# Kernel tuning notes

Measured on AMD Instinct MI355X. Metric: run time of the kernel, lower is better.

## Reference

```python
import jax, jax.numpy as jnp
import numpy as np

B, S, H = 4096, 15, 1024
PQ, CFG = 1003, 128
IN = PQ + 5 + 10 + 3 + 3  # 1024, matches input_size in torch module
EPS = 1e-5


def lstm_cell(x, h, c, Wih, Whh, bih, bhh):
    # PyTorch LSTMCell gate order: i, f, g, o
    gates = x @ Wih.T + bih + h @ Whh.T + bhh
    i, f, g, o = jnp.split(gates, 4, axis=-1)
    c2 = jax.nn.sigmoid(f) * c + jax.nn.sigmoid(i) * jnp.tanh(g)
    h2 = jax.nn.sigmoid(o) * jnp.tanh(c2)
    return h2, c2


def setup_inputs() -> dict:
    key = jax.random.key(0)
    ks = jax.random.split(key, 16)
    g = lambda i, shape, s=0.02: jax.random.normal(ks[i], shape, jnp.float32) * s
    u = lambda i, shape: jax.random.uniform(ks[i], shape, jnp.float32, -1.0, 1.0)
    return {
        "input_p_q": jax.random.normal(ks[0], (B, S, PQ), jnp.float32),
        "input_config": jax.random.normal(ks[1], (B, S, CFG), jnp.float32),
        "input_time": jax.random.randint(ks[2], (B, S, 3), 0, 5),
        "W_cfg": g(3, (10, CFG)), "b_cfg": jnp.zeros((10,), jnp.float32),
        "emb_hour": g(4, (24, 5), 1.0),
        "emb_weekday": g(5, (8, 3), 1.0),
        "emb_season": g(6, (5, 3), 1.0),
        # init(): uniform(-1,1) weights, zero bias for the two attention layers
        "W_sa": u(7, (IN, IN + 2 * H)), "b_sa": jnp.zeros((IN,), jnp.float32),
        "Wih_s": g(8, (4 * H, IN)), "Whh_s": g(9, (4 * H, H)),
        "bih_s": jnp.zeros((4 * H,), jnp.float32), "bhh_s": jnp.zeros((4 * H,), jnp.float32),
        "Wih_t": g(10, (4 * H, H)), "Whh_t": g(11, (4 * H, H)),
        "bih_t": jnp.zeros((4 * H,), jnp.float32), "bhh_t": jnp.zeros((4 * H,), jnp.float32),
        "W_ta": u(12, (1, 3 * H)), "b_ta": jnp.zeros((1,), jnp.float32),
        "bn_gamma": jnp.ones((S,), jnp.float32), "bn_beta": jnp.zeros((S,), jnp.float32),
        "Wih_d": g(13, (4, H)), "Whh_d": g(14, (4, 1)),
        "bih_d": jnp.zeros((4,), jnp.float32), "bhh_d": jnp.zeros((4,), jnp.float32),
    }


def reference(input_p_q, input_config, input_time,
              W_cfg, b_cfg, emb_hour, emb_weekday, emb_season,
              W_sa, b_sa, Wih_s, Whh_s, bih_s, bhh_s,
              Wih_t, Whh_t, bih_t, bhh_t, W_ta, b_ta,
              bn_gamma, bn_beta, Wih_d, Whh_d, bih_d, bhh_d):
    cfg = input_config @ W_cfg.T + b_cfg                       # [B,S,10]
    hr = emb_hour[input_time[:, :, 0]]                         # [B,S,5]
    wd = emb_weekday[input_time[:, :, 1]]                      # [B,S,3]
    sn = emb_season[input_time[:, :, 2]]                       # [B,S,3]
    inputs = jnp.concatenate([input_p_q, cfg, hr, wd, sn], axis=2)  # [B,S,IN]

    Bsz, Ssz = inputs.shape[0], inputs.shape[1]
    Hd = Whh_s.shape[1]
    h0 = jnp.zeros((Bsz, Hd), inputs.dtype)

    # ---- spatial encoder with per-step attention gating ----
    def step1(carry, x):
        h, c = carry
        score = jnp.tanh(jnp.concatenate([h, c, x], axis=1) @ W_sa.T + b_sa)
        h2, c2 = lstm_cell(x * score, h, c, Wih_s, Whh_s, bih_s, bhh_s)
        return (h2, c2), h2

    _, mid = jax.lax.scan(step1, (h0, h0), jnp.swapaxes(inputs, 0, 1))  # [S,B,H]
    mid = jnp.swapaxes(mid, 0, 1)                                      # [B,S,H]

    # ---- BatchNorm1d(15) in training mode: channels = sequence dim ----
    mu = mid.mean(axis=(0, 2), keepdims=True)
    var = mid.var(axis=(0, 2), keepdims=True)  # biased variance, as torch uses for normalization
    mid = (mid - mu) * jax.lax.rsqrt(var + EPS) * bn_gamma[None, :, None] + bn_beta[None, :, None]

    # ---- temporal encoder with post-step attention score ----
    def step2(carry, x):
        h, c = carry
        h2, c2 = lstm_cell(x, h, c, Wih_t, Whh_t, bih_t, bhh_t)
        att = jnp.tanh(jnp.concatenate([h2, c2, x], axis=1) @ W_ta.T + b_ta)  # [B,1]
        return (h2, c2), (h2, att)

    _, (outs, att2) = jax.lax.scan(step2, (h0, h0), jnp.swapaxes(mid, 0, 1))
    outs = jnp.swapaxes(outs, 0, 1)   # [B,S,H]
    att2 = jnp.swapaxes(att2, 0, 1)   # [B,S,1]

    # ---- decoder nn.LSTM (batch_first=False!) scans over the BATCH axis ----
    hd0 = jnp.zeros((Ssz, 1), outs.dtype)

    def step3(carry, x):
        h, c = carry
        h2, c2 = lstm_cell(x, h, c, Wih_d, Whh_d, bih_d, bhh_d)
        return (h2, c2), h2

    _, out1d = jax.lax.scan(step3, (hd0, hd0), outs)  # [B,S,1]

    sm = jax.nn.softmax(att2, axis=1)  # [B,S,1]
    # bmm(out1d^T [B,1,S], sm [B,S,1]) -> [B,1,1]
    out = jnp.einsum('bs,bs->b', out1d[:, :, 0], sm[:, :, 0])[:, None, None]
    return out
```

## Files before the change

kernel.cpp:

```cpp
#include <hip/hip_runtime.h>

#define AS1 __attribute__((address_space(1)))
#define AS3 __attribute__((address_space(3)))

typedef __attribute__((ext_vector_type(8))) _Float16 f16x8;
typedef __attribute__((ext_vector_type(4))) float f32x4;

static constexpr int BATCH = 4096;
static constexpr int SEQ   = 15;

__device__ __forceinline__ float h2f(unsigned short u) {
  return (float)__builtin_bit_cast(_Float16, u);
}
__device__ __forceinline__ unsigned short f2h(float f) {
  return __builtin_bit_cast(unsigned short, (_Float16)f);
}
__device__ __forceinline__ float frcp(float x) { return __builtin_amdgcn_rcpf(x); }
__device__ __forceinline__ float sigm(float x)  { return frcp(1.0f + __expf(-x)); }
__device__ __forceinline__ float tanhx(float x) { return 1.0f - 2.0f * frcp(1.0f + __expf(2.0f * x)); }

template<int STAGE>
__global__ __launch_bounds__(512, 2)
void gemm_lstm256(const unsigned short* A0, int lda0, int K0,
                  const unsigned short* A1, int lda1,
                  const unsigned short* Bw, int K,
                  const float* ib, float* Cst,
                  unsigned short* P0, unsigned short* P1, unsigned short* P2,
                  float* F0)
{
  __shared__ unsigned short lds[2][2][16384];
  const int tid  = threadIdx.x;
  const int wid  = tid >> 6;
  const int lane = tid & 63;
  const int wr = wid >> 2;
  const int wc = wid & 3;
  const int NT = K >> 6;

  const int bid = blockIdx.y * gridDim.x + blockIdx.x;
  const int cpx = (gridDim.x * gridDim.y) >> 3;
  const int swz = (bid & 7) * cpx + (bid >> 3);
  const int row0 = (swz / gridDim.x) * 256;
  const int col0 = (swz % gridDim.x) * 256;

  auto stage_half = [&](int bb, int mat, int hh, int kt) {
    const int k0 = kt * 64;
    const unsigned short* Ap; int lda, kc, rb;
    if (mat == 0) {
      if (k0 < K0) { Ap = A0; lda = lda0; kc = k0; }
      else         { Ap = A1; lda = lda1; kc = k0 - K0; }
      rb = row0;
    } else { Ap = Bw; lda = K; kc = k0; rb = col0; }
#pragma unroll
    for (int i = 0; i < 2; ++i) {
      const int x  = (tid + i * 512) * 16;
      const int xs = x ^ (((x >> 9) & 1) << 5);
      const int r  = hh * 128 + (xs >> 7);
      const int cb = xs & 127;
      const unsigned short* src = Ap + (size_t)(rb + r) * lda + kc + (cb >> 1);
      __builtin_amdgcn_global_load_lds((const AS1 void*)src,
          (AS3 void*)((char*)&lds[bb][mat][0] + hh * 16384 + wid * 1024 + i * 8192),
          16, 0, 0);
    }
  };

  const int frow = lane & 15;
  const int axor = ((lane >> 2) & 1) << 5;
  const int abase = ((((wr * 128 + frow) << 7) + (((lane >> 4) & 3) << 4))) ^ axor;
  const int bbase = ((((wc * 64  + frow) << 7) + (((lane >> 4) & 3) << 4))) ^ axor;

  const f32x4 zero = {0.f, 0.f, 0.f, 0.f};
  f32x4 acc[8][4];
#pragma unroll
  for (int i = 0; i < 8; ++i)
#pragma unroll
    for (int j = 0; j < 4; ++j) acc[i][j] = zero;

  stage_half(0, 0, 0, 0);
  stage_half(0, 0, 1, 0);
  stage_half(0, 1, 0, 0);
  stage_half(0, 1, 1, 0);
  if (NT > 1) { stage_half(1, 1, 0, 1); stage_half(1, 1, 1, 1); }
  asm volatile("s_waitcnt vmcnt(4)" ::: "memory");
  __builtin_amdgcn_s_barrier();

#define DO_PHASE(MB, STG, VMW)                                                        \
  {                                                                                   \
    const f16x8 a0 = *(const f16x8*)(ldsA + abase + (MB)     * 2048);                 \
    const f16x8 a1 = *(const f16x8*)(ldsA + abase + (MB)     * 2048 + 64);            \
    const f16x8 a2 = *(const f16x8*)(ldsA + abase + (MB + 1) * 2048);                 \
    const f16x8 a3 = *(const f16x8*)(ldsA + abase + (MB + 1) * 2048 + 64);            \
    STG;                                                                              \
    __builtin_amdgcn_s_barrier();                                                     \
    asm volatile("s_waitcnt lgkmcnt(0)" ::: "memory");                                \
    __builtin_amdgcn_sched_barrier(0);                                                \
    __builtin_amdgcn_s_setprio(1);                                                    \
    _Pragma("unroll")                                                                 \
    for (int n = 0; n < 4; ++n) {                                                     \
      acc[MB][n]     = __builtin_amdgcn_mfma_f32_16x16x32_f16(a0, bv[n][0], acc[MB][n],     0, 0, 0); \
      acc[MB][n]     = __builtin_amdgcn_mfma_f32_16x16x32_f16(a1, bv[n][1], acc[MB][n],     0, 0, 0); \
      acc[MB + 1][n] = __builtin_amdgcn_mfma_f32_16x16x32_f16(a2, bv[n][0], acc[MB + 1][n], 0, 0, 0); \
      acc[MB + 1][n] = __builtin_amdgcn_mfma_f32_16x16x32_f16(a3, bv[n][1], acc[MB + 1][n], 0, 0, 0); \
    }                                                                                 \
    __builtin_amdgcn_s_setprio(0);                                                    \
    VMW;                                                                              \
    __builtin_amdgcn_s_barrier();                                                     \
  }

  for (int kt = 0; kt < NT; ++kt) {
    const int cur = kt & 1;
    const char* ldsA = (const char*)&lds[cur][0][0];
    const char* ldsB = (const char*)&lds[cur][1][0];
    f16x8 bv[4][2];
#pragma unroll
    for (int n = 0; n < 4; ++n) {
      bv[n][0] = *(const f16x8*)(ldsB + bbase + n * 2048);
      bv[n][1] = *(const f16x8*)(ldsB + bbase + n * 2048 + 64);
    }
    DO_PHASE(0, { if (kt + 1 < NT) stage_half(cur ^ 1, 0, 0, kt + 1); }, { (void)0; });
    DO_PHASE(2, { if (kt + 1 < NT) stage_half(cur ^ 1, 0, 1, kt + 1); }, { (void)0; });
    DO_PHASE(4, { if (kt + 2 < NT) stage_half(cur,     1, 0, kt + 2); }, { (void)0; });
    DO_PHASE(6, { if (kt + 2 < NT) stage_half(cur,     1, 1, kt + 2); },
             { if (kt >= NT - 2) { asm volatile("s_waitcnt vmcnt(0)" ::: "memory"); }
               else              { asm volatile("s_waitcnt vmcnt(4)" ::: "memory"); } });
  }
#undef DO_PHASE

  __syncthreads();
  char* base = (char*)&lds[0][0][0];
  unsigned short* hS = (unsigned short*)base;
  unsigned short* cS = (unsigned short*)(base + 32768);
  float*          hF = (float*)base;
  float* xw = (float*)(base + 65536) + wid * 256;

  const int cs = lane & 3;
  const int er = (lane >> 4) << 2;
  const int uq = (lane >> 2) & 3;

  float cold[8][4];
#pragma unroll
  for (int mi = 0; mi < 8; ++mi)
#pragma unroll
    for (int ni = 0; ni < 4; ++ni) {
      const int R = row0 + wr * 128 + mi * 16 + er + cs;
      const int U = ((col0 + wc * 64 + ni * 16) >> 2) + uq;
      cold[mi][ni] = Cst[(size_t)R * 1024 + U];
    }

#pragma unroll
  for (int mi = 0; mi < 8; ++mi)
#pragma unroll
    for (int ni = 0; ni < 4; ++ni) {
      __builtin_amdgcn_wave_barrier();
      *(f32x4*)(xw + lane * 4) = acc[mi][ni];
      __builtin_amdgcn_wave_barrier();
      __builtin_amdgcn_sched_barrier(0);
      const int qb = (lane & 60) * 4;
      const float g0 = xw[qb + 0  + cs];
      const float g1 = xw[qb + 4  + cs];
      const float g2 = xw[qb + 8  + cs];
      const float g3 = xw[qb + 12 + cs];
      __builtin_amdgcn_wave_barrier();
      const int R = row0 + wr * 128 + mi * 16 + er + cs;
      const int U = ((col0 + wc * 64 + ni * 16) >> 2) + uq;
      const f32x4 b4 = *(const f32x4*)(ib + 4 * U);
      const float gi = g0 + b4[0];
      const float gf = g1 + b4[1];
      const float gg = g2 + b4[2];
      const float go = g3 + b4[3];
      const float cn = sigm(gf) * cold[mi][ni] + sigm(gi) * tanhx(gg);
      const float hn = sigm(go) * tanhx(cn);
      Cst[(size_t)R * 1024 + U] = cn;
      const int Rl = wr * 128 + mi * 16 + er + cs;
      const int Ul = wc * 16 + ni * 4 + uq;
      if (STAGE == 1) {
        hS[Rl * 64 + Ul] = f2h(hn);
        cS[Rl * 64 + Ul] = f2h(cn);
      } else {
        hF[Rl * 64 + Ul] = hn;
      }
    }
  __syncthreads();

  const int U0 = col0 >> 2;
  if (STAGE == 1) {
#pragma unroll
    for (int it = 0; it < 4; ++it) {
      const int idx = it * 512 + tid;
      const int r = idx >> 3, o = idx & 7;
      const int4 hv = *(const int4*)((char*)hS + idx * 16);
      const int4 cv = *(const int4*)((char*)cS + idx * 16);
      *(int4*)(P0 + (size_t)(row0 + r) * 2048 + U0 + o * 8)        = hv;
      *(int4*)(P0 + (size_t)(row0 + r) * 2048 + 1024 + U0 + o * 8) = cv;
      *(int4*)(P1 + (size_t)(row0 + r) * 2048 + 1024 + U0 + o * 8) = hv;
      *(int4*)(P2 + (size_t)(row0 + r) * 1024 + U0 + o * 8)        = hv;
    }
  } else {
#pragma unroll
    for (int it = 0; it < 8; ++it) {
      const int idx = it * 512 + tid;
      const int r = idx >> 4, o = idx & 15;
      const f32x4 hv = *(const f32x4*)((char*)hF + idx * 16);
      *(f32x4*)(F0 + (size_t)(row0 + r) * 1024 + U0 + o * 4) = hv;
      uint2 pk;
      pk.x = (unsigned)f2h(hv[0]) | ((unsigned)f2h(hv[1]) << 16);
      pk.y = (unsigned)f2h(hv[2]) | ((unsigned)f2h(hv[3]) << 16);
      *(uint2*)(P0 + (size_t)(row0 + r) * 1024 + U0 + o * 4) = pk;
    }
  }
}

__global__ __launch_bounds__(256, 2)
void gemm_score2ph(const unsigned short* A0, int lda0, int K0,
                   const unsigned short* A1, int lda1,
                   const unsigned short* Bw, int K,
                   const float* bias, const unsigned short* X,
                   unsigned short* OutG)
{
  __shared__ unsigned short lds[2][12288];
  const int tid  = threadIdx.x;
  const int wid  = tid >> 6;
  const int lane = tid & 63;
  const int wr = wid >> 1;
  const int wc = wid & 1;
  const int NT = K >> 6;

  const int bid = blockIdx.y * gridDim.x + blockIdx.x;
  const int cpx = (gridDim.x * gridDim.y) >> 3;
  const int swz = (bid & 7) * cpx + (bid >> 3);
  const int row0 = (swz / gridDim.x) * 128;
  const int col0 = (swz % gridDim.x) * 64;

  auto stage_A = [&](int bb, int kt) {
    const int k0 = kt * 64;
    const unsigned short* Ap; int lda, kc;
    if (k0 < K0) { Ap = A0; lda = lda0; kc = k0; }
    else         { Ap = A1; lda = lda1; kc = k0 - K0; }
#pragma unroll
    for (int i = 0; i < 4; ++i) {
      const int x  = (i * 256 + tid) * 16;
      const int xs = x ^ (((x >> 9) & 1) << 5);
      const int r  = xs >> 7;
      const int cb = xs & 127;
      const unsigned short* src = Ap + (size_t)(row0 + r) * lda + kc + (cb >> 1);
      __builtin_amdgcn_global_load_lds((const AS1 void*)src,
          (AS3 void*)((char*)&lds[bb][0] + i * 4096 + wid * 1024), 16, 0, 0);
    }
  };
  auto stage_B = [&](int bb, int kt) {
    const int k0 = kt * 64;
#pragma unroll
    for (int i = 0; i < 2; ++i) {
      const int x  = (i * 256 + tid) * 16;
      const int xs = x ^ (((x >> 9) & 1) << 5);
      const int r  = xs >> 7;
      const int cb = xs & 127;
      const unsigned short* src = Bw + (size_t)(col0 + r) * K + k0 + (cb >> 1);
      __builtin_amdgcn_global_load_lds((const AS1 void*)src,
          (AS3 void*)((char*)&lds[bb][0] + 16384 + i * 4096 + wid * 1024), 16, 0, 0);
    }
  };

  const int frow = lane & 15;
  const int axor = ((lane >> 2) & 1) << 5;
  const int abase = ((((wr * 64 + frow) << 7) + ((lane >> 4) << 4))) ^ axor;
  const int bbase = ((((wc * 32 + frow) << 7) + ((lane >> 4) << 4))) ^ axor;

  const f32x4 zero = {0.f, 0.f, 0.f, 0.f};
  f32x4 acc[4][2];
#pragma unroll
  for (int i = 0; i < 4; ++i)
#pragma unroll
    for (int j = 0; j < 2; ++j) acc[i][j] = zero;

  stage_A(0, 0);
  stage_B(0, 0);
  if (NT > 1) stage_B(1, 1);
  asm volatile("s_waitcnt vmcnt(2)" ::: "memory");
  __builtin_amdgcn_s_barrier();

  for (int kt = 0; kt < NT; ++kt) {
    const int cur = kt & 1;
    const char* ldsA = (const char*)&lds[cur][0];
    const char* ldsB = ldsA + 16384;
    f16x8 bv[2][2];
#pragma unroll
    for (int n = 0; n < 2; ++n) {
      bv[n][0] = *(const f16x8*)(ldsB + bbase + n * 2048);
      bv[n][1] = *(const f16x8*)(ldsB + bbase + n * 2048 + 64);
    }
    f16x8 a00 = *(const f16x8*)(ldsA + abase);
    f16x8 a01 = *(const f16x8*)(ldsA + abase + 64);
    f16x8 a10 = *(const f16x8*)(ldsA + abase + 2048);
    f16x8 a11 = *(const f16x8*)(ldsA + abase + 2048 + 64);
    if (kt + 1 < NT) stage_A(cur ^ 1, kt + 1);
    __builtin_amdgcn_s_barrier();
    asm volatile("s_waitcnt lgkmcnt(0)" ::: "memory");
    __builtin_amdgcn_sched_barrier(0);
    __builtin_amdgcn_s_setprio(1);
#pragma unroll
    for (int n = 0; n < 2; ++n) {
      acc[0][n] = __builtin_amdgcn_mfma_f32_16x16x32_f16(a00, bv[n][0], acc[0][n], 0, 0, 0);
      acc[0][n] = __builtin_amdgcn_mfma_f32_16x16x32_f16(a01, bv[n][1], acc[0][n], 0, 0, 0);
      acc[1][n] = __builtin_amdgcn_mfma_f32_16x16x32_f16(a10, bv[n][0], acc[1][n], 0, 0, 0);
      acc[1][n] = __builtin_amdgcn_mfma_f32_16x16x32_f16(a11, bv[n][1], acc[1][n], 0, 0, 0);
    }
    __builtin_amdgcn_s_setprio(0);
    __builtin_amdgcn_s_barrier();
    f16x8 a20 = *(const f16x8*)(ldsA + abase + 2 * 2048);
    f16x8 a21 = *(const f16x8*)(ldsA + abase + 2 * 2048 + 64);
    f16x8 a30 = *(const f16x8*)(ldsA + abase + 3 * 2048);
    f16x8 a31 = *(const f16x8*)(ldsA + abase + 3 * 2048 + 64);
    if (kt + 2 < NT) stage_B(cur, kt + 2);
    __builtin_amdgcn_s_barrier();
    asm volatile("s_waitcnt lgkmcnt(0)" ::: "memory");
    __builtin_amdgcn_sched_barrier(0);
    __builtin_amdgcn_s_setprio(1);
#pragma unroll
    for (int n = 0; n < 2; ++n) {
      acc[2][n] = __builtin_amdgcn_mfma_f32_16x16x32_f16(a20, bv[n][0], acc[2][n], 0, 0, 0);
      acc[2][n] = __builtin_amdgcn_mfma_f32_16x16x32_f16(a21, bv[n][1], acc[2][n], 0, 0, 0);
      acc[3][n] = __builtin_amdgcn_mfma_f32_16x16x32_f16(a30, bv[n][0], acc[3][n], 0, 0, 0);
      acc[3][n] = __builtin_amdgcn_mfma_f32_16x16x32_f16(a31, bv[n][1], acc[3][n], 0, 0, 0);
    }
    __builtin_amdgcn_s_setprio(0);
    if (kt >= NT - 2) { asm volatile("s_waitcnt vmcnt(0)" ::: "memory"); }
    else              { asm volatile("s_waitcnt vmcnt(2)" ::: "memory"); }
    __builtin_amdgcn_s_barrier();
  }

  const int er = (lane >> 4) << 2;
#pragma unroll
  for (int mi = 0; mi < 4; ++mi)
#pragma unroll
    for (int ni = 0; ni < 2; ++ni) {
      const int row = row0 + wr * 64 + mi * 16 + er;
      const int col = col0 + wc * 32 + ni * 16 + frow;
      const float bs = bias[col];
#pragma unroll
      for (int r = 0; r < 4; ++r) {
        const float v = tanhx(acc[mi][ni][r] + bs);
        const float xv = h2f(X[(size_t)(row + r) * 1024 + col]);
        OutG[(size_t)(row + r) * 2048 + col] = f2h(xv * v);
      }
    }
}

__global__ void f2h_copy(const float* src, unsigned short* dst, int n) {
  const int i = blockIdx.x * 256 + threadIdx.x;
  if (i < n) dst[i] = f2h(src[i]);
}

__global__ void cat_w_int(const float* wih, const float* whh, unsigned short* dst) {
  const int i = blockIdx.x * 256 + threadIdx.x;
  const int n = i >> 11, k = i & 2047;
  const int u = n >> 2, g = n & 3;
  const int src = g * 1024 + u;
  dst[i] = f2h(k < 1024 ? wih[src * 1024 + k] : whh[src * 1024 + (k - 1024)]);
}

__global__ void prep_bias(const float* bih, const float* bhh, float* ib) {
  const int i = blockIdx.x * 256 + threadIdx.x;
  const int u = i >> 2, g = i & 3;
  ib[i] = bih[g * 1024 + u] + bhh[g * 1024 + u];
}

__global__ void copy_pq(const float* pq, unsigned short* inb) {
  const int i4 = blockIdx.x * 256 + threadIdx.x;
  const float4 v = ((const float4*)pq)[i4];
  const int base = i4 * 4;
  const float vv[4] = {v.x, v.y, v.z, v.w};
#pragma unroll
  for (int e = 0; e < 4; ++e) {
    const int idx = base + e;
    const int bt = idx / 1003;
    const int j = idx - bt * 1003;
    const int b = bt / 15;
    const int t = bt - b * 15;
    inb[((size_t)t * BATCH + b) * 1024 + j] = f2h(vv[e]);
  }
}

__global__ void cfg_emb(const float* cfg, const int* tim,
                        const float* Wc, const float* bc,
                        const float* eh, const float* ew, const float* es,
                        unsigned short* inb)
{
  const int wv = (blockIdx.x * 256 + threadIdx.x) >> 6;
  const int lane = threadIdx.x & 63;
  const int b = wv / 15, t = wv - b * 15;
  const float* cp = cfg + (size_t)wv * 128;
  const float c0 = cp[lane], c1v = cp[lane + 64];
  unsigned short* dst = inb + ((size_t)t * BATCH + b) * 1024;
#pragma unroll
  for (int g = 0; g < 10; ++g) {
    float v = fmaf(c0, Wc[g * 128 + lane], c1v * Wc[g * 128 + 64 + lane]);
    v += __shfl_xor(v, 32); v += __shfl_xor(v, 16); v += __shfl_xor(v, 8);
    v += __shfl_xor(v, 4);  v += __shfl_xor(v, 2);  v += __shfl_xor(v, 1);
    if (lane == 0) dst[1003 + g] = f2h(v + bc[g]);
  }
  if (lane < 5)       dst[1013 + lane] = f2h(eh[tim[wv * 3 + 0] * 5 + lane]);
  else if (lane < 8)  dst[1018 + (lane - 5)] = f2h(ew[tim[wv * 3 + 1] * 3 + (lane - 5)]);
  else if (lane < 11) dst[1021 + (lane - 8)] = f2h(es[tim[wv * 3 + 2] * 3 + (lane - 8)]);
}

__global__ void bn_partial(const unsigned short* mid, float* part) {
  const int t = blockIdx.y, blk = blockIdx.x, tid = threadIdx.x;
  const unsigned short* p = mid + (size_t)t * BATCH * 1024;
  float s = 0.f, ss = 0.f;
  for (int i = blk * 256 + tid; i < BATCH * 1024; i += 128 * 256) {
    const float v = h2f(p[i]);
    s += v; ss += v * v;
  }
  for (int o = 32; o > 0; o >>= 1) { s += __shfl_down(s, o); ss += __shfl_down(ss, o); }
  __shared__ float sm[8];
  if ((tid & 63) == 0) { sm[(tid >> 6) * 2] = s; sm[(tid >> 6) * 2 + 1] = ss; }
  __syncthreads();
  if (tid == 0) {
    part[(t * 128 + blk) * 2]     = sm[0] + sm[2] + sm[4] + sm[6];
    part[(t * 128 + blk) * 2 + 1] = sm[1] + sm[3] + sm[5] + sm[7];
  }
}

__global__ void bn_final(const float* part, const float* gamma, const float* beta, float* scsh) {
  const int t = blockIdx.x, tid = threadIdx.x;
  float s = part[(t * 128 + tid) * 2], ss = part[(t * 128 + tid) * 2 + 1];
  for (int o = 32; o > 0; o >>= 1) { s += __shfl_down(s, o); ss += __shfl_down(ss, o); }
  __shared__ float sm[4];
  if ((tid & 63) == 0) { sm[(tid >> 6) * 2] = s; sm[(tid >> 6) * 2 + 1] = ss; }
  __syncthreads();
  if (tid == 0) {
    const float S = sm[0] + sm[2], SS = sm[1] + sm[3];
    const float inv = 1.f / (float)(BATCH * 1024);
    const float mu = S * inv;
    const float var = SS * inv - mu * mu;
    const float rstd = rsqrtf(var + 1e-5f);
    const float sc = rstd * gamma[t];
    scsh[t * 2] = sc;
    scsh[t * 2 + 1] = beta[t] - mu * sc;
  }
}

__global__ void bn_apply(unsigned short* mid, const float* scsh) {
  const int t = blockIdx.y;
  const int i = blockIdx.x * 256 + threadIdx.x;
  unsigned short* p = mid + (size_t)t * BATCH * 1024;
  p[i] = f2h(h2f(p[i]) * scsh[t * 2] + scsh[t * 2 + 1]);
}

__global__ void att_proj(const float* h2, const float* c2, const unsigned short* xn,
                         const float* Wta, const float* bta, const float* Wihd,
                         float* att2, float* proj, int t)
{
  const int b = blockIdx.x, tid = threadIdx.x;
  const float* h = h2 + (size_t)b * 1024;
  const float* c = c2 + (size_t)b * 1024;
  const unsigned short* x = xn + (size_t)b * 1024;
  float a = 0.f, p0 = 0.f, p1 = 0.f, p2 = 0.f, p3 = 0.f;
  for (int j = tid; j < 1024; j += 256) {
    const float hv = h[j], cv = c[j], xv = h2f(x[j]);
    a  += hv * Wta[j] + cv * Wta[1024 + j] + xv * Wta[2048 + j];
    p0 += hv * Wihd[j];
    p1 += hv * Wihd[1024 + j];
    p2 += hv * Wihd[2048 + j];
    p3 += hv * Wihd[3072 + j];
  }
  for (int o = 32; o > 0; o >>= 1) {
    a  += __shfl_down(a, o);  p0 += __shfl_down(p0, o); p1 += __shfl_down(p1, o);
    p2 += __shfl_down(p2, o); p3 += __shfl_down(p3, o);
  }
  __shared__ float sm[4][5];
  if ((tid & 63) == 0) {
    const int w = tid >> 6;
    sm[w][0] = a; sm[w][1] = p0; sm[w][2] = p1; sm[w][3] = p2; sm[w][4] = p3;
  }
  __syncthreads();
  if (tid == 0) {
    att2[b * SEQ + t] = tanhx(sm[0][0] + sm[1][0] + sm[2][0] + sm[3][0] + bta[0]);
    float* pp = proj + ((size_t)b * SEQ + t) * 4;
    pp[0] = sm[0][1] + sm[1][1] + sm[2][1] + sm[3][1];
    pp[1] = sm[0][2] + sm[1][2] + sm[2][2] + sm[3][2];
    pp[2] = sm[0][3] + sm[1][3] + sm[2][3] + sm[3][3];
    pp[3] = sm[0][4] + sm[1][4] + sm[2][4] + sm[3][4];
  }
}

__global__ __launch_bounds__(256) void lstm3_par(
    const float* proj, const float* Whhd,
    const float* bihd, const float* bhhd, float* out1d)
{
  const int s = blockIdx.x;
  const int tid = threadIdx.x;
  constexpr int CH = BATCH / 256;
  const float wi = Whhd[0], wf = Whhd[1], wg = Whhd[2], wo = Whhd[3];
  const float bi = bihd[0] + bhhd[0], bf_ = bihd[1] + bhhd[1];
  const float bg = bihd[2] + bhhd[2], bo = bihd[3] + bhhd[3];
  const float4* p4 = (const float4*)proj;
  float4 p[CH];
#pragma unroll
  for (int u = 0; u < CH; ++u) p[u] = p4[(tid * CH + u) * SEQ + s];
  __shared__ float Hb[257], Cb[257];
  Hb[tid] = 0.f; Cb[tid] = 0.f;
  if (tid == 255) { Hb[256] = 0.f; Cb[256] = 0.f; }
  __syncthreads();
  float h, c;
  for (int it = 0; it < 8; ++it) {
    h = Hb[tid]; c = Cb[tid];
#pragma unroll
    for (int u = 0; u < CH; ++u) {
      const float gi = fmaf(h, wi, p[u].x + bi);
      const float gf = fmaf(h, wf, p[u].y + bf_);
      const float gg = fmaf(h, wg, p[u].z + bg);
      const float go = fmaf(h, wo, p[u].w + bo);
      c = sigm(gf) * c + sigm(gi) * tanhx(gg);
      h = sigm(go) * tanhx(c);
    }
    __syncthreads();
    Hb[tid + 1] = h; Cb[tid + 1] = c;
    __syncthreads();
  }
  h = Hb[tid]; c = Cb[tid];
#pragma unroll
  for (int u = 0; u < CH; ++u) {
    const float gi = fmaf(h, wi, p[u].x + bi);
    const float gf = fmaf(h, wf, p[u].y + bf_);
    const float gg = fmaf(h, wg, p[u].z + bg);
    const float go = fmaf(h, wo, p[u].w + bo);
    c = sigm(gf) * c + sigm(gi) * tanhx(gg);
    h = sigm(go) * tanhx(c);
    out1d[(tid * CH + u) * SEQ + s] = h;
  }
}

__global__ void finalize_k(const float* att2, const float* out1d, float* out) {
  const int b = blockIdx.x * 64 + threadIdx.x;
  const float* a = att2 + b * SEQ;
  const float* o = out1d + b * SEQ;
  float m = -1e30f;
  for (int s = 0; s < SEQ; ++s) m = fmaxf(m, a[s]);
  float den = 0.f, num = 0.f;
  for (int s = 0; s < SEQ; ++s) {
    const float e = __expf(a[s] - m);
    den += e; num += e * o[s];
  }
  out[b] = num / den;
}

extern "C" void kernel_launch(void* const* d_in, const int* in_sizes, int n_in,
                              void* d_out, int out_size, void* d_ws, size_t ws_size,
                              hipStream_t stream)
{
  (void)in_sizes; (void)n_in; (void)out_size; (void)ws_size;
  const float* in_pq   = (const float*)d_in[0];
  const float* in_cfg  = (const float*)d_in[1];
  const int*   in_time = (const int*)d_in[2];
  const float* W_cfg   = (const float*)d_in[3];
  const float* b_cfg   = (const float*)d_in[4];
  const float* emb_h   = (const float*)d_in[5];
  const float* emb_w   = (const float*)d_in[6];
  const float* emb_s   = (const float*)d_in[7];
  const float* W_sa    = (const float*)d_in[8];
  const float* b_sa    = (const float*)d_in[9];
  const float* Wih_s   = (const float*)d_in[10];
  const float* Whh_s   = (const float*)d_in[11];
  const float* bih_s   = (const float*)d_in[12];
  const float* bhh_s   = (const float*)d_in[13];
  const float* Wih_t   = (const float*)d_in[14];
  const float* Whh_t   = (const float*)d_in[15];
  const float* bih_t   = (const float*)d_in[16];
  const float* bhh_t   = (const float*)d_in[17];
  const float* W_ta    = (const float*)d_in[18];
  const float* b_ta    = (const float*)d_in[19];
  const float* gamma   = (const float*)d_in[20];
  const float* beta    = (const float*)d_in[21];
  const float* Wih_d   = (const float*)d_in[22];
  const float* Whh_d   = (const float*)d_in[23];
  const float* bih_d   = (const float*)d_in[24];
  const float* bhh_d   = (const float*)d_in[25];
  float* out = (float*)d_out;

  char* w = (char*)d_ws;
  size_t off = 0;
  auto alloc = [&](size_t bytes) -> char* {
    char* p = w + off;
    off = (off + bytes + 255) & ~(size_t)255;
    return p;
  };
  unsigned short* inb  = (unsigned short*)alloc((size_t)SEQ * BATCH * 1024 * 2);
  unsigned short* hc   = (unsigned short*)alloc((size_t)BATCH * 2048 * 2);
  unsigned short* gA0  = (unsigned short*)alloc((size_t)BATCH * 2048 * 2);
  unsigned short* gA1  = (unsigned short*)alloc((size_t)BATCH * 2048 * 2);
  float*          c1   = (float*)alloc((size_t)BATCH * 1024 * 4);
  unsigned short* h2b0 = (unsigned short*)alloc((size_t)BATCH * 1024 * 2);
  unsigned short* h2b1 = (unsigned short*)alloc((size_t)BATCH * 1024 * 2);
  float*          h2f_ = (float*)alloc((size_t)BATCH * 1024 * 4);
  float*          c2f  = (float*)alloc((size_t)BATCH * 1024 * 4);
  unsigned short* wsab = (unsigned short*)alloc((size_t)1024 * 3072 * 2);
  unsigned short* w1   = (unsigned short*)alloc((size_t)4096 * 2048 * 2);
  unsigned short* w2   = (unsigned short*)alloc((size_t)4096 * 2048 * 2);
  float*          ib1  = (float*)alloc(4096 * 4);
  float*          ib2  = (float*)alloc(4096 * 4);
  float*          part = (float*)alloc(15 * 128 * 2 * 4);
  float*          scsh = (float*)alloc(15 * 2 * 4);
  float*          att2 = (float*)alloc((size_t)BATCH * SEQ * 4);
  float*          proj = (float*)alloc((size_t)BATCH * SEQ * 4 * 4);
  float*          o1d  = (float*)alloc((size_t)BATCH * SEQ * 4);

  unsigned short* gAbuf[2]  = {gA0, gA1};
  unsigned short* h2bbuf[2] = {h2b0, h2b1};

  hipMemsetAsync(hc,   0, (size_t)BATCH * 2048 * 2, stream);
  hipMemsetAsync(gA0,  0, (size_t)BATCH * 2048 * 2, stream);
  hipMemsetAsync(c1,   0, (size_t)BATCH * 1024 * 4, stream);
  hipMemsetAsync(h2b0, 0, (size_t)BATCH * 1024 * 2, stream);
  hipMemsetAsync(c2f,  0, (size_t)BATCH * 1024 * 4, stream);

  f2h_copy<<<(1024 * 3072) / 256, 256, 0, stream>>>(W_sa, wsab, 1024 * 3072);
  cat_w_int<<<(4096 * 2048) / 256, 256, 0, stream>>>(Wih_s, Whh_s, w1);
  cat_w_int<<<(4096 * 2048) / 256, 256, 0, stream>>>(Wih_t, Whh_t, w2);
  prep_bias<<<16, 256, 0, stream>>>(bih_s, bhh_s, ib1);
  prep_bias<<<16, 256, 0, stream>>>(bih_t, bhh_t, ib2);
  copy_pq<<<(BATCH * SEQ * 1003 / 4) / 256, 256, 0, stream>>>(in_pq, inb);
  cfg_emb<<<(BATCH * SEQ) / 4, 256, 0, stream>>>(in_cfg, in_time, W_cfg, b_cfg,
                                                 emb_h, emb_w, emb_s, inb);

  for (int t = 0; t < SEQ; ++t) {
    unsigned short* xt = inb + (size_t)t * BATCH * 1024;
    gemm_score2ph<<<dim3(1024 / 64, BATCH / 128), 256, 0, stream>>>(
        hc, 2048, 2048, xt, 1024, wsab, 3072, b_sa, xt, gAbuf[t & 1]);
    gemm_lstm256<1><<<dim3(4096 / 256, BATCH / 256), 512, 0, stream>>>(
        gAbuf[t & 1], 2048, 2048, gAbuf[t & 1], 2048, w1, 2048,
        ib1, c1, hc, gAbuf[(t + 1) & 1], xt, nullptr);
  }

  bn_partial<<<dim3(128, SEQ), 256, 0, stream>>>(inb, part);
  bn_final<<<SEQ, 128, 0, stream>>>(part, gamma, beta, scsh);
  bn_apply<<<dim3((BATCH * 1024) / 256, SEQ), 256, 0, stream>>>(inb, scsh);

  for (int t = 0; t < SEQ; ++t) {
    const unsigned short* xt = inb + (size_t)t * BATCH * 1024;
    gemm_lstm256<2><<<dim3(4096 / 256, BATCH / 256), 512, 0, stream>>>(
        xt, 1024, 1024, h2bbuf[t & 1], 1024, w2, 2048,
        ib2, c2f, h2bbuf[(t + 1) & 1], nullptr, nullptr, h2f_);
    att_proj<<<BATCH, 256, 0, stream>>>(h2f_, c2f, xt, W_ta, b_ta, Wih_d, att2, proj, t);
  }

  lstm3_par<<<SEQ, 256, 0, stream>>>(proj, Whh_d, bih_d, bhh_d, o1d);
  finalize_k<<<BATCH / 64, 64, 0, stream>>>(att2, o1d, out);
}
```

Baseline: 3.544 ms.

## Fuse attention score and decoder projection dot products into temporal LSTM epilogue

The stage-2 LSTM GEMM epilogue now computes per-row partial dot products of h and c with the attention weights and the decoder input weights while the values are still in registers. It writes these 16 column-block partials to a buffer instead of storing an fp32 copy of h. A single reduction kernel after the loop sums them, and a separate batched kernel precomputes the x·W_ta term across all timesteps. This removes the per-step att_proj kernel, which reread fp32 h and c from global memory, at the cost of extra epilogue work, LDS use and partial-sum storage.

```diff
diff --git a/kernel.cpp b/kernel.cpp
--- a/kernel.cpp
+++ b/kernel.cpp
@@ -26,7 +26,7 @@
                   const unsigned short* Bw, int K,
                   const float* ib, float* Cst,
                   unsigned short* P0, unsigned short* P1, unsigned short* P2,
-                  float* F0)
+                  const float* Wta, const float* Wihd, float* redG)
 {
   __shared__ unsigned short lds[2][2][16384];
   const int tid  = threadIdx.x;
@@ -127,14 +127,10 @@
 
   __syncthreads();
   char* base = (char*)&lds[0][0][0];
-  unsigned short* hS = (unsigned short*)base;
-  unsigned short* cS = (unsigned short*)(base + 32768);
-  float*          hF = (float*)base;
-  float* xw = (float*)(base + 65536) + wid * 256;
-
   const int cs = lane & 3;
   const int er = (lane >> 4) << 2;
   const int uq = (lane >> 2) & 3;
+  const int U0g = col0 >> 2;
 
   float cold[8][4];
 #pragma unroll
@@ -142,69 +138,127 @@
 #pragma unroll
     for (int ni = 0; ni < 4; ++ni) {
       const int R = row0 + wr * 128 + mi * 16 + er + cs;
-      const int U = ((col0 + wc * 64 + ni * 16) >> 2) + uq;
+      const int U = U0g + wc * 16 + ni * 4 + uq;
       cold[mi][ni] = Cst[(size_t)R * 1024 + U];
     }
 
-#pragma unroll
-  for (int mi = 0; mi < 8; ++mi)
-#pragma unroll
-    for (int ni = 0; ni < 4; ++ni) {
-      __builtin_amdgcn_wave_barrier();
-      *(f32x4*)(xw + lane * 4) = acc[mi][ni];
-      __builtin_amdgcn_wave_barrier();
-      __builtin_amdgcn_sched_barrier(0);
-      const int qb = (lane & 60) * 4;
-      const float g0 = xw[qb + 0  + cs];
-      const float g1 = xw[qb + 4  + cs];
-      const float g2 = xw[qb + 8  + cs];
-      const float g3 = xw[qb + 12 + cs];
-      __builtin_amdgcn_wave_barrier();
-      const int R = row0 + wr * 128 + mi * 16 + er + cs;
-      const int U = ((col0 + wc * 64 + ni * 16) >> 2) + uq;
-      const f32x4 b4 = *(const f32x4*)(ib + 4 * U);
-      const float gi = g0 + b4[0];
-      const float gf = g1 + b4[1];
-      const float gg = g2 + b4[2];
-      const float go = g3 + b4[3];
-      const float cn = sigm(gf) * cold[mi][ni] + sigm(gi) * tanhx(gg);
-      const float hn = sigm(go) * tanhx(cn);
-      Cst[(size_t)R * 1024 + U] = cn;
-      const int Rl = wr * 128 + mi * 16 + er + cs;
-      const int Ul = wc * 16 + ni * 4 + uq;
-      if (STAGE == 1) {
+  if constexpr (STAGE == 1) {
+    unsigned short* hS = (unsigned short*)base;
+    unsigned short* cS = (unsigned short*)(base + 32768);
+    float* xw = (float*)(base + 65536) + wid * 256;
+#pragma unroll
+    for (int mi = 0; mi < 8; ++mi)
+#pragma unroll
+      for (int ni = 0; ni < 4; ++ni) {
+        __builtin_amdgcn_wave_barrier();
+        *(f32x4*)(xw + lane * 4) = acc[mi][ni];
+        __builtin_amdgcn_wave_barrier();
+        __builtin_amdgcn_sched_barrier(0);
+        const int qb = (lane & 60) * 4;
+        const float g0 = xw[qb + 0  + cs];
+        const float g1 = xw[qb + 4  + cs];
+        const float g2 = xw[qb + 8  + cs];
+        const float g3 = xw[qb + 12 + cs];
+        __builtin_amdgcn_wave_barrier();
+        const int R = row0 + wr * 128 + mi * 16 + er + cs;
+        const int U = U0g + wc * 16 + ni * 4 + uq;
+        const f32x4 b4 = *(const f32x4*)(ib + 4 * U);
+        const float cn = sigm(g1 + b4[1]) * cold[mi][ni]
+                       + sigm(g0 + b4[0]) * tanhx(g2 + b4[2]);
+        const float hn = sigm(g3 + b4[3]) * tanhx(cn);
+        Cst[(size_t)R * 1024 + U] = cn;
+        const int Rl = wr * 128 + mi * 16 + er + cs;
+        const int Ul = wc * 16 + ni * 4 + uq;
         hS[Rl * 64 + Ul] = f2h(hn);
         cS[Rl * 64 + Ul] = f2h(cn);
-      } else {
-        hF[Rl * 64 + Ul] = hn;
       }
-    }
-  __syncthreads();
-
-  const int U0 = col0 >> 2;
-  if (STAGE == 1) {
+    __syncthreads();
 #pragma unroll
     for (int it = 0; it < 4; ++it) {
       const int idx = it * 512 + tid;
       const int r = idx >> 3, o = idx & 7;
       const int4 hv = *(const int4*)((char*)hS + idx * 16);
       const int4 cv = *(const int4*)((char*)cS + idx * 16);
-      *(int4*)(P0 + (size_t)(row0 + r) * 2048 + U0 + o * 8)        = hv;
-      *(int4*)(P0 + (size_t)(row0 + r) * 2048 + 1024 + U0 + o * 8) = cv;
-      *(int4*)(P1 + (size_t)(row0 + r) * 2048 + 1024 + U0 + o * 8) = hv;
-      *(int4*)(P2 + (size_t)(row0 + r) * 1024 + U0 + o * 8)        = hv;
+      *(int4*)(P0 + (size_t)(row0 + r) * 2048 + U0g + o * 8)        = hv;
+      *(int4*)(P0 + (size_t)(row0 + r) * 2048 + 1024 + U0g + o * 8) = cv;
+      *(int4*)(P1 + (size_t)(row0 + r) * 2048 + 1024 + U0g + o * 8) = hv;
+      *(int4*)(P2 + (size_t)(row0 + r) * 1024 + U0g + o * 8)        = hv;
     }
   } else {
-#pragma unroll
-    for (int it = 0; it < 8; ++it) {
+    unsigned short* hS = (unsigned short*)base;
+    float* xw  = (float*)(base + 32768) + wid * 256;
+    float* wL  = (float*)(base + 40960);
+    float* red = (float*)(base + 49152);
+    if (tid < 64) {
+      wL[tid]       = Wta[U0g + tid];
+      wL[64 + tid]  = Wta[1024 + U0g + tid];
+      wL[128 + tid] = Wihd[U0g + tid];
+      wL[192 + tid] = Wihd[1024 + U0g + tid];
+      wL[256 + tid] = Wihd[2048 + U0g + tid];
+      wL[320 + tid] = Wihd[3072 + U0g + tid];
+    }
+    __syncthreads();
+    float aH[8] = {}, q0[8] = {}, q1[8] = {}, q2[8] = {}, q3[8] = {};
+#pragma unroll
+    for (int mi = 0; mi < 8; ++mi)
+#pragma unroll
+      for (int ni = 0; ni < 4; ++ni) {
+        __builtin_amdgcn_wave_barrier();
+        *(f32x4*)(xw + lane * 4) = acc[mi][ni];
+        __builtin_amdgcn_wave_barrier();
+        __builtin_amdgcn_sched_barrier(0);
+        const int qb = (lane & 60) * 4;
+        const float g0 = xw[qb + 0  + cs];
+        const float g1 = xw[qb + 4  + cs];
+        const float g2 = xw[qb + 8  + cs];
+        const float g3 = xw[qb + 12 + cs];
+        __builtin_amdgcn_wave_barrier();
+        const int R = row0 + wr * 128 + mi * 16 + er + cs;
+        const int U = U0g + wc * 16 + ni * 4 + uq;
+        const f32x4 b4 = *(const f32x4*)(ib + 4 * U);
+        const float cn = sigm(g1 + b4[1]) * cold[mi][ni]
+                       + sigm(g0 + b4[0]) * tanhx(g2 + b4[2]);
+        const float hn = sigm(g3 + b4[3]) * tanhx(cn);
+        Cst[(size_t)R * 1024 + U] = cn;
+        const int Rl = wr * 128 + mi * 16 + er + cs;
+        const int ul = wc * 16 + ni * 4 + uq;
+        hS[Rl * 64 + ul] = f2h(hn);
+        aH[mi] = fmaf(hn, wL[ul], fmaf(cn, wL[64 + ul], aH[mi]));
+        q0[mi] = fmaf(hn, wL[128 + ul], q0[mi]);
+        q1[mi] = fmaf(hn, wL[192 + ul], q1[mi]);
+        q2[mi] = fmaf(hn, wL[256 + ul], q2[mi]);
+        q3[mi] = fmaf(hn, wL[320 + ul], q3[mi]);
+      }
+#pragma unroll
+    for (int mi = 0; mi < 8; ++mi) {
+      aH[mi] += __shfl_xor(aH[mi], 4); aH[mi] += __shfl_xor(aH[mi], 8);
+      q0[mi] += __shfl_xor(q0[mi], 4); q0[mi] += __shfl_xor(q0[mi], 8);
+      q1[mi] += __shfl_xor(q1[mi], 4); q1[mi] += __shfl_xor(q1[mi], 8);
+      q2[mi] += __shfl_xor(q2[mi], 4); q2[mi] += __shfl_xor(q2[mi], 8);
+      q3[mi] += __shfl_xor(q3[mi], 4); q3[mi] += __shfl_xor(q3[mi], 8);
+    }
+    if (uq == 0) {
+#pragma unroll
+      for (int mi = 0; mi < 8; ++mi) {
+        const int r = wr * 128 + mi * 16 + er + cs;
+        float* d = red + ((size_t)wc * 256 + r) * 5;
+        d[0] = aH[mi]; d[1] = q0[mi]; d[2] = q1[mi]; d[3] = q2[mi]; d[4] = q3[mi];
+      }
+    }
+    __syncthreads();
+    const int cb = col0 >> 8;
+    for (int idx = tid; idx < 1280; idx += 512) {
+      const int r = idx / 5, k = idx - r * 5;
+      const float s = red[(0 * 256 + r) * 5 + k] + red[(1 * 256 + r) * 5 + k]
+                    + red[(2 * 256 + r) * 5 + k] + red[(3 * 256 + r) * 5 + k];
+      redG[((size_t)(row0 + r) * 16 + cb) * 5 + k] = s;
+    }
+#pragma unroll
+    for (int it = 0; it < 4; ++it) {
       const int idx = it * 512 + tid;
-      const int r = idx >> 4, o = idx & 15;
-      const f32x4 hv = *(const f32x4*)((char*)hF + idx * 16);
-      *(f32x4*)(F0 + (size_t)(row0 + r) * 1024 + U0 + o * 4) = hv;
-      uint2 pk;
-      pk.x = (unsigned)f2h(hv[0]) | ((unsigned)f2h(hv[1]) << 16);
-      pk.y = (unsigned)f2h(hv[2]) | ((unsigned)f2h(hv[3]) << 16);
-      *(uint2*)(P0 + (size_t)(row0 + r) * 1024 + U0 + o * 4) = pk;
+      const int r = idx >> 3, o = idx & 7;
+      const int4 hv = *(const int4*)((char*)hS + idx * 16);
+      *(int4*)(P0 + (size_t)(row0 + r) * 1024 + U0g + o * 8) = hv;
     }
   }
 }
@@ -447,41 +501,38 @@
   p[i] = f2h(h2f(p[i]) * scsh[t * 2] + scsh[t * 2 + 1]);
 }
 
-__global__ void att_proj(const float* h2, const float* c2, const unsigned short* xn,
-                         const float* Wta, const float* bta, const float* Wihd,
-                         float* att2, float* proj, int t)
-{
-  const int b = blockIdx.x, tid = threadIdx.x;
-  const float* h = h2 + (size_t)b * 1024;
-  const float* c = c2 + (size_t)b * 1024;
-  const unsigned short* x = xn + (size_t)b * 1024;
-  float a = 0.f, p0 = 0.f, p1 = 0.f, p2 = 0.f, p3 = 0.f;
-  for (int j = tid; j < 1024; j += 256) {
-    const float hv = h[j], cv = c[j], xv = h2f(x[j]);
-    a  += hv * Wta[j] + cv * Wta[1024 + j] + xv * Wta[2048 + j];
-    p0 += hv * Wihd[j];
-    p1 += hv * Wihd[1024 + j];
-    p2 += hv * Wihd[2048 + j];
-    p3 += hv * Wihd[3072 + j];
-  }
-  for (int o = 32; o > 0; o >>= 1) {
-    a  += __shfl_down(a, o);  p0 += __shfl_down(p0, o); p1 += __shfl_down(p1, o);
-    p2 += __shfl_down(p2, o); p3 += __shfl_down(p3, o);
-  }
-  __shared__ float sm[4][5];
-  if ((tid & 63) == 0) {
-    const int w = tid >> 6;
-    sm[w][0] = a; sm[w][1] = p0; sm[w][2] = p1; sm[w][3] = p2; sm[w][4] = p3;
-  }
-  __syncthreads();
-  if (tid == 0) {
-    att2[b * SEQ + t] = tanhx(sm[0][0] + sm[1][0] + sm[2][0] + sm[3][0] + bta[0]);
-    float* pp = proj + ((size_t)b * SEQ + t) * 4;
-    pp[0] = sm[0][1] + sm[1][1] + sm[2][1] + sm[3][1];
-    pp[1] = sm[0][2] + sm[1][2] + sm[2][2] + sm[3][2];
-    pp[2] = sm[0][3] + sm[1][3] + sm[2][3] + sm[3][3];
-    pp[3] = sm[0][4] + sm[1][4] + sm[2][4] + sm[3][4];
-  }
+__global__ void xdot_k(const unsigned short* xn, const float* Wta, float* xdot) {
+  const int wv = (blockIdx.x * 256 + threadIdx.x) >> 6;
+  const int lane = threadIdx.x & 63;
+  const unsigned short* x = xn + (size_t)wv * 1024;
+  const float* wx = Wta + 2048 + lane * 16;
+  const f16x8 v0 = ((const f16x8*)x)[lane * 2];
+  const f16x8 v1 = ((const f16x8*)x)[lane * 2 + 1];
+  float s = 0.f;
+#pragma unroll
+  for (int e = 0; e < 8; ++e) s = fmaf((float)v0[e], wx[e], s);
+#pragma unroll
+  for (int e = 0; e < 8; ++e) s = fmaf((float)v1[e], wx[8 + e], s);
+  s += __shfl_xor(s, 32); s += __shfl_xor(s, 16); s += __shfl_xor(s, 8);
+  s += __shfl_xor(s, 4);  s += __shfl_xor(s, 2);  s += __shfl_xor(s, 1);
+  if (lane == 0) xdot[wv] = s;
+}
+
+__global__ void att_reduce(const float* redT, const float* xdot, const float* bta,
+                           float* att2, float* proj) {
+  const int i = blockIdx.x * 256 + threadIdx.x;
+  const int t = i >> 12;
+  const int b = i & 4095;
+  const float* p = redT + (size_t)i * 80;
+  float s0 = 0.f, s1 = 0.f, s2 = 0.f, s3 = 0.f, s4 = 0.f;
+#pragma unroll
+  for (int cb = 0; cb < 16; ++cb) {
+    s0 += p[cb * 5 + 0]; s1 += p[cb * 5 + 1]; s2 += p[cb * 5 + 2];
+    s3 += p[cb * 5 + 3]; s4 += p[cb * 5 + 4];
+  }
+  att2[b * SEQ + t] = tanhx(s0 + xdot[i] + bta[0]);
+  float* pp = proj + ((size_t)b * SEQ + t) * 4;
+  pp[0] = s1; pp[1] = s2; pp[2] = s3; pp[3] = s4;
 }
 
 __global__ __launch_bounds__(256) void lstm3_par(
@@ -592,7 +643,6 @@
   float*          c1   = (float*)alloc((size_t)BATCH * 1024 * 4);
   unsigned short* h2b0 = (unsigned short*)alloc((size_t)BATCH * 1024 * 2);
   unsigned short* h2b1 = (unsigned short*)alloc((size_t)BATCH * 1024 * 2);
-  float*          h2f_ = (float*)alloc((size_t)BATCH * 1024 * 4);
   float*          c2f  = (float*)alloc((size_t)BATCH * 1024 * 4);
   unsigned short* wsab = (unsigned short*)alloc((size_t)1024 * 3072 * 2);
   unsigned short* w1   = (unsigned short*)alloc((size_t)4096 * 2048 * 2);
@@ -604,6 +654,8 @@
   float*          att2 = (float*)alloc((size_t)BATCH * SEQ * 4);
   float*          proj = (float*)alloc((size_t)BATCH * SEQ * 4 * 4);
   float*          o1d  = (float*)alloc((size_t)BATCH * SEQ * 4);
+  float*          redT = (float*)alloc((size_t)SEQ * BATCH * 16 * 5 * 4);
+  float*          xdot = (float*)alloc((size_t)SEQ * BATCH * 4);
 
   unsigned short* gAbuf[2]  = {gA0, gA1};
   unsigned short* h2bbuf[2] = {h2b0, h2b1};
@@ -629,20 +681,22 @@
         hc, 2048, 2048, xt, 1024, wsab, 3072, b_sa, xt, gAbuf[t & 1]);
     gemm_lstm256<1><<<dim3(4096 / 256, BATCH / 256), 512, 0, stream>>>(
         gAbuf[t & 1], 2048, 2048, gAbuf[t & 1], 2048, w1, 2048,
-        ib1, c1, hc, gAbuf[(t + 1) & 1], xt, nullptr);
+        ib1, c1, hc, gAbuf[(t + 1) & 1], xt, nullptr, nullptr, nullptr);
   }
 
   bn_partial<<<dim3(128, SEQ), 256, 0, stream>>>(inb, part);
   bn_final<<<SEQ, 128, 0, stream>>>(part, gamma, beta, scsh);
   bn_apply<<<dim3((BATCH * 1024) / 256, SEQ), 256, 0, stream>>>(inb, scsh);
+  xdot_k<<<(SEQ * BATCH * 64) / 256, 256, 0, stream>>>(inb, W_ta, xdot);
 
   for (int t = 0; t < SEQ; ++t) {
     const unsigned short* xt = inb + (size_t)t * BATCH * 1024;
     gemm_lstm256<2><<<dim3(4096 / 256, BATCH / 256), 512, 0, stream>>>(
         xt, 1024, 1024, h2bbuf[t & 1], 1024, w2, 2048,
-        ib2, c2f, h2bbuf[(t + 1) & 1], nullptr, nullptr, h2f_);
-    att_proj<<<BATCH, 256, 0, stream>>>(h2f_, c2f, xt, W_ta, b_ta, Wih_d, att2, proj, t);
-  }
+        ib2, c2f, h2bbuf[(t + 1) & 1], nullptr, nullptr,
+        W_ta, Wih_d, redT + (size_t)t * BATCH * 80);
+  }
+  att_reduce<<<(SEQ * BATCH) / 256, 256, 0, stream>>>(redT, xdot, b_ta, att2, proj);
 
   lstm3_par<<<SEQ, 256, 0, stream>>>(proj, Whh_d, bih_d, bhh_d, o1d);
   finalize_k<<<BATCH / 64, 64, 0, stream>>>(att2, o1d, out);
```

Result: faster. 3.434 ms (-3.1%).
